# Kernel optimization log

Measured on AMD Instinct MI355X. Metric: run time of the kernel, lower is better.

Reference implementation:

```python
import jax, jax.numpy as jnp
import numpy as np

N_POINTS = 8192
N_TOPICS = 64
B = 524288


def setup_inputs() -> dict:
    key = jax.random.key(0)
    k1, k2, k3, k4 = jax.random.split(key, 4)
    pij = jax.random.uniform(k1, (B,), dtype=jnp.float32, minval=1e-6, maxval=1.0)
    i = jax.random.randint(k2, (B,), 0, N_POINTS, dtype=jnp.int64)
    j = jax.random.randint(k3, (B,), 0, N_POINTS, dtype=jnp.int64)
    W = jax.random.normal(k4, (N_POINTS, N_TOPICS), dtype=jnp.float32)  # nn.Embedding weight
    return {"pij": pij, "i": i, "j": j, "W": W}


def reference(pij, i, j, W):
    # pairwise squared distances over ALL points, via the gram trick
    # (avoids materializing the [n, n, d] broadcasted tensor of the torch code)
    sq = jnp.sum(W * W, axis=1)                       # [n]
    d2 = sq[:, None] + sq[None, :] - 2.0 * (W @ W.T)  # [n, n]
    d2 = jnp.maximum(d2, 0.0)                         # numerical floor (exact math is >= 0)
    n = W.shape[0]
    # Cauchy kernel partition: sum_{k,l} 1/(1+d2) minus the n diagonal ones
    part = jnp.sum(1.0 / (1.0 + d2)) - jnp.asarray(n, d2.dtype)
    xi = W[i]                                         # [B, d]
    xj = W[j]                                         # [B, d]
    # FAITHFUL to source: (1 + diff^2).sum(1) adds 1 per dim => n_topics + ||xi-xj||^2
    num = 1.0 / jnp.sum(1.0 + (xi - xj) ** 2, axis=1)  # [B]
    qij = num / part
    loss_kld = pij * (jnp.log(pij) - jnp.log(qij))
    return jnp.sum(loss_kld)
```

## Files before the change

kernel.cpp:

```cpp
#include <hip/hip_runtime.h>
#include <math.h>

#define NPOINTS   8192
#define NDIM      64
#define TILE      128
#define NT2       64
#define NBLK      2080
#define NPAIRB    1040
#define NPW       (NPAIRB * 4)
#define GRID      3120

#define WS_W16   0
#define WS_SQ    262144
#define WS_PARTA 270336
#define WS_A1P   272416
#define WS_A3P   273456

typedef __attribute__((ext_vector_type(8))) short bf16x8;
typedef __attribute__((ext_vector_type(4))) float f32x4;

__device__ inline unsigned short f2bf(float f) {
    unsigned u = __float_as_uint(f);
    u += 0x7FFFu + ((u >> 16) & 1u);
    return (unsigned short)(u >> 16);
}
__device__ inline float bflo(unsigned u) { return __uint_as_float(u << 16); }
__device__ inline float bfhi(unsigned u) { return __uint_as_float(u & 0xFFFF0000u); }

__global__ __launch_bounds__(256) void prep_kernel(const float* __restrict__ W,
                                                   float* __restrict__ sq,
                                                   unsigned* __restrict__ W16) {
    int wid  = (blockIdx.x * 256 + threadIdx.x) >> 6;
    int lane = threadIdx.x & 63;
    float v = W[wid * NDIM + lane];
    float s = v * v;
    #pragma unroll
    for (int m = 32; m >= 1; m >>= 1) s += __shfl_xor(s, m, 64);
    if (lane == 0) sq[wid] = s;
    unsigned bf   = f2bf(v);
    unsigned peer = (unsigned)__shfl_xor((int)bf, 1, 64);
    if ((lane & 1) == 0)
        W16[wid * 32 + (lane >> 1)] = (bf & 0xFFFFu) | (peer << 16);
}

__global__ __launch_bounds__(256) void fused_kernel(const unsigned* __restrict__ W16,
                                                    const float* __restrict__ sq,
                                                    const float* __restrict__ pij,
                                                    const int* __restrict__ ii,
                                                    const int* __restrict__ jj,
                                                    int nb,
                                                    float* __restrict__ partA,
                                                    float* __restrict__ a1p,
                                                    float* __restrict__ a3p) {
    __shared__ float red[8];
    int zb = blockIdx.x;
    int t = threadIdx.x, w = t >> 6, lane = t & 63;

    if ((zb % 3) < 2) {
        int z = (zb / 3) * 2 + (zb % 3);
        int by = (int)((129.0 - sqrt(16641.0 - 8.0 * (double)z)) * 0.5);
        while (by * NT2 - by * (by - 1) / 2 > z) --by;
        while ((by + 1) * NT2 - (by + 1) * by / 2 <= z) ++by;
        int bx = by + (z - (by * NT2 - by * (by - 1) / 2));

        int wm = w >> 1, wn = w & 1, quad = lane >> 4, l15 = lane & 15;
        int a0 = by * TILE, b0 = bx * TILE;

        float4 base1[4];
        float  sqb[4];
        {
            int arow = a0 + wm * 64 + quad * 4;
            #pragma unroll
            for (int tm = 0; tm < 4; ++tm) {
                float4 v = *(const float4*)(sq + arow + tm * 16);
                base1[tm] = (float4){1.0f + v.x, 1.0f + v.y, 1.0f + v.z, 1.0f + v.w};
            }
            int bcol = b0 + wn * 64 + l15;
            #pragma unroll
            for (int tn = 0; tn < 4; ++tn) sqb[tn] = sq[bcol + tn * 16];
        }

        f32x4 acc[4][4];
        #pragma unroll
        for (int i = 0; i < 4; ++i)
            #pragma unroll
            for (int j = 0; j < 4; ++j) acc[i][j] = (f32x4){0.f, 0.f, 0.f, 0.f};

        const unsigned* Arow = W16 + (a0 + wm * 64 + l15) * 32;
        const unsigned* Brow = W16 + (b0 + wn * 64 + l15) * 32;
        #pragma unroll
        for (int h = 0; h < 2; ++h) {
            bf16x8 af[4], bfr[4];
            #pragma unroll
            for (int tm = 0; tm < 4; ++tm)
                af[tm] = *(const bf16x8*)(Arow + tm * 16 * 32 + h * 16 + quad * 4);
            #pragma unroll
            for (int tn = 0; tn < 4; ++tn)
                bfr[tn] = *(const bf16x8*)(Brow + tn * 16 * 32 + h * 16 + quad * 4);
            #pragma unroll
            for (int tm = 0; tm < 4; ++tm)
                #pragma unroll
                for (int tn = 0; tn < 4; ++tn)
                    acc[tm][tn] = __builtin_amdgcn_mfma_f32_16x16x32_bf16(af[tm], bfr[tn],
                                                                          acc[tm][tn], 0, 0, 0);
        }

        float ssum = 0.f;
        if (bx > by) {
            #pragma unroll
            for (int tn = 0; tn < 4; ++tn) {
                float c0 = sqb[tn];
                #pragma unroll
                for (int tm = 0; tm < 4; ++tm) {
                    ssum += __builtin_amdgcn_rcpf(fmaf(acc[tm][tn][0], -2.0f, base1[tm].x + c0));
                    ssum += __builtin_amdgcn_rcpf(fmaf(acc[tm][tn][1], -2.0f, base1[tm].y + c0));
                    ssum += __builtin_amdgcn_rcpf(fmaf(acc[tm][tn][2], -2.0f, base1[tm].z + c0));
                    ssum += __builtin_amdgcn_rcpf(fmaf(acc[tm][tn][3], -2.0f, base1[tm].w + c0));
                }
            }
        } else {
            int quad4 = quad * 4;
            #pragma unroll
            for (int tn = 0; tn < 4; ++tn) {
                int cl = wn * 64 + tn * 16 + l15;
                float c0 = sqb[tn];
                float b4[4];
                #pragma unroll
                for (int tm = 0; tm < 4; ++tm) {
                    b4[0] = base1[tm].x; b4[1] = base1[tm].y;
                    b4[2] = base1[tm].z; b4[3] = base1[tm].w;
                    #pragma unroll
                    for (int r = 0; r < 4; ++r) {
                        int rl = wm * 64 + tm * 16 + quad4 + r;
                        float inv = __builtin_amdgcn_rcpf(fmaf(acc[tm][tn][r], -2.0f, b4[r] + c0));
                        ssum += (cl > rl) ? inv : 0.f;
                    }
                }
            }
        }
        #pragma unroll
        for (int m = 32; m >= 1; m >>= 1) ssum += __shfl_xor(ssum, m, 64);
        if (lane == 0) red[w] = ssum;
        __syncthreads();
        if (t == 0) partA[z] = red[0] + red[1] + red[2] + red[3];
    } else {
        int pb = zb / 3;
        int pw = pb * 4 + w;
        int g = lane >> 3;
        int s = lane & 7;
        float a1 = 0.f, a3 = 0.f;

        #pragma unroll 2
        for (int p0 = pw * 16; p0 < nb; p0 += NPW * 16) {
            int  pA = p0 + g,        pB = p0 + 8 + g;
            bool okA = pA < nb,      okB = pB < nb;
            int  cA = okA ? pA : 0,  cB = okB ? pB : 0;
            int   iA = ii[cA], jA = jj[cA];
            int   iB = ii[cB], jB = jj[cB];
            float pvA = pij[cA], pvB = pij[cB];
            uint4 xiA = *(const uint4*)(W16 + iA * 32 + s * 4);
            uint4 xjA = *(const uint4*)(W16 + jA * 32 + s * 4);
            uint4 xiB = *(const uint4*)(W16 + iB * 32 + s * 4);
            uint4 xjB = *(const uint4*)(W16 + jB * 32 + s * 4);
            float sA = sq[iA] + sq[jA];
            float sB = sq[iB] + sq[jB];

            float dA, dB;
            {
                dA = bflo(xiA.x) * bflo(xjA.x);
                dA = fmaf(bfhi(xiA.x), bfhi(xjA.x), dA);
                dA = fmaf(bflo(xiA.y), bflo(xjA.y), dA);
                dA = fmaf(bfhi(xiA.y), bfhi(xjA.y), dA);
                dA = fmaf(bflo(xiA.z), bflo(xjA.z), dA);
                dA = fmaf(bfhi(xiA.z), bfhi(xjA.z), dA);
                dA = fmaf(bflo(xiA.w), bflo(xjA.w), dA);
                dA = fmaf(bfhi(xiA.w), bfhi(xjA.w), dA);
            }
            {
                dB = bflo(xiB.x) * bflo(xjB.x);
                dB = fmaf(bfhi(xiB.x), bfhi(xjB.x), dB);
                dB = fmaf(bflo(xiB.y), bflo(xjB.y), dB);
                dB = fmaf(bfhi(xiB.y), bfhi(xjB.y), dB);
                dB = fmaf(bflo(xiB.z), bflo(xjB.z), dB);
                dB = fmaf(bfhi(xiB.z), bfhi(xjB.z), dB);
                dB = fmaf(bflo(xiB.w), bflo(xjB.w), dB);
                dB = fmaf(bfhi(xiB.w), bfhi(xjB.w), dB);
            }
            #pragma unroll
            for (int m = 1; m <= 4; m <<= 1) {
                dA += __shfl_xor(dA, m, 64);
                dB += __shfl_xor(dB, m, 64);
            }
            float vA = fmaf(dA, -2.0f, sA);
            float vB = fmaf(dB, -2.0f, sB);
            float tA = pvA * __logf(pvA * ((float)NDIM + vA));
            float tB = pvB * __logf(pvB * ((float)NDIM + vB));
            a1 += okA ? tA : 0.f;  a3 += okA ? pvA : 0.f;
            a1 += okB ? tB : 0.f;  a3 += okB ? pvB : 0.f;
        }
        #pragma unroll
        for (int m = 32; m >= 1; m >>= 1) {
            a1 += __shfl_xor(a1, m, 64);
            a3 += __shfl_xor(a3, m, 64);
        }
        if (lane == 0) { red[w] = a1 * 0.125f; red[4 + w] = a3 * 0.125f; }
        __syncthreads();
        if (t == 0) {
            a1p[pb] = red[0] + red[1] + red[2] + red[3];
            a3p[pb] = red[4] + red[5] + red[6] + red[7];
        }
    }
}

__global__ __launch_bounds__(256) void final_kernel(const float* __restrict__ partA,
                                                    const float* __restrict__ a1p,
                                                    const float* __restrict__ a3p,
                                                    float* __restrict__ out) {
    __shared__ double r1[256], r2[256], r3[256];
    int t = threadIdx.x;
    double dpart = 0.0, d1 = 0.0, d3 = 0.0;
    for (int k = t; k < NBLK; k += 256) dpart += (double)partA[k];
    for (int k = t; k < NPAIRB; k += 256) { d1 += (double)a1p[k]; d3 += (double)a3p[k]; }
    r1[t] = dpart; r2[t] = d1; r3[t] = d3;
    __syncthreads();
    for (int s = 128; s >= 1; s >>= 1) {
        if (t < s) { r1[t] += r1[t + s]; r2[t] += r2[t + s]; r3[t] += r3[t + s]; }
        __syncthreads();
    }
    if (t == 0) {
        double part = 2.0 * r1[0];
        out[0] = (float)(r2[0] + r3[0] * log(part));
    }
}

extern "C" void kernel_launch(void* const* d_in, const int* in_sizes, int n_in,
                              void* d_out, int out_size, void* d_ws, size_t ws_size,
                              hipStream_t stream) {
    const float* pij = (const float*)d_in[0];
    const int*   ii  = (const int*)d_in[1];
    const int*   jj  = (const int*)d_in[2];
    const float* W   = (const float*)d_in[3];
    float* out = (float*)d_out;
    float* ws  = (float*)d_ws;

    unsigned* W16   = (unsigned*)ws + WS_W16;
    float*    sqv   = ws + WS_SQ;
    float*    partA = ws + WS_PARTA;
    float*    a1p   = ws + WS_A1P;
    float*    a3p   = ws + WS_A3P;

    int nb = in_sizes[0];

    prep_kernel<<<NPOINTS / 4, 256, 0, stream>>>(W, sqv, W16);
    fused_kernel<<<GRID, 256, 0, stream>>>(W16, sqv, pij, ii, jj, nb, partA, a1p, a3p);
    final_kernel<<<1, 256, 0, stream>>>(partA, a1p, a3p, out);
}
```

Measured before the change: 110.9 us.

## Gather embeddings as fp8 and compute direct squared differences for pair loss

The prep kernel now also packs W into fp8 (e4m3) rows. The pair branch gathers 8-byte fp8 chunks instead of 16-byte bf16 ones and computes the sum of squared differences directly, which drops the sq lookups and the gram-trick subtraction. The block interleave changes from 2:1 to 1:1, doubling the number of pair blocks to spread the gather work. This halves the gather bytes per pair, but fp8 precision is coarse and may push the loss sum outside tolerance.

```diff
diff --git a/kernel.cpp b/kernel.cpp
--- a/kernel.cpp
+++ b/kernel.cpp
@@ -6,32 +6,38 @@
 #define TILE      128
 #define NT2       64
 #define NBLK      2080
-#define NPAIRB    1040
+#define NPAIRB    2080
 #define NPW       (NPAIRB * 4)
-#define GRID      3120
+#define GRID      (NBLK + NPAIRB)
 
 #define WS_W16   0
-#define WS_SQ    262144
-#define WS_PARTA 270336
-#define WS_A1P   272416
-#define WS_A3P   273456
+#define WS_W8    262144
+#define WS_SQ    393216
+#define WS_PARTA 401408
+#define WS_A1P   403488
+#define WS_A3P   405568
 
 typedef __attribute__((ext_vector_type(8))) short bf16x8;
 typedef __attribute__((ext_vector_type(4))) float f32x4;
+typedef __attribute__((ext_vector_type(2))) float f32x2;
 
 __device__ inline unsigned short f2bf(float f) {
     unsigned u = __float_as_uint(f);
     u += 0x7FFFu + ((u >> 16) & 1u);
     return (unsigned short)(u >> 16);
 }
-__device__ inline float bflo(unsigned u) { return __uint_as_float(u << 16); }
-__device__ inline float bfhi(unsigned u) { return __uint_as_float(u & 0xFFFF0000u); }
+template <bool HI>
+__device__ inline f32x2 cvt2(unsigned dw) {
+    return __builtin_amdgcn_cvt_pk_f32_fp8((int)dw, HI);
+}
 
 __global__ __launch_bounds__(256) void prep_kernel(const float* __restrict__ W,
                                                    float* __restrict__ sq,
-                                                   unsigned* __restrict__ W16) {
-    int wid  = (blockIdx.x * 256 + threadIdx.x) >> 6;
-    int lane = threadIdx.x & 63;
+                                                   unsigned* __restrict__ W16,
+                                                   unsigned* __restrict__ W8) {
+    int t    = threadIdx.x;
+    int wid  = (blockIdx.x * 256 + t) >> 6;
+    int lane = t & 63;
     float v = W[wid * NDIM + lane];
     float s = v * v;
     #pragma unroll
@@ -41,9 +47,16 @@
     unsigned peer = (unsigned)__shfl_xor((int)bf, 1, 64);
     if ((lane & 1) == 0)
         W16[wid * 32 + (lane >> 1)] = (bf & 0xFFFFu) | (peer << 16);
+    if (t < 64) {
+        float4 x = *(const float4*)(W + blockIdx.x * 256 + t * 4);
+        int lo = __builtin_amdgcn_cvt_pk_fp8_f32(x.x, x.y, 0, false);
+        int dw = __builtin_amdgcn_cvt_pk_fp8_f32(x.z, x.w, lo, true);
+        W8[blockIdx.x * 64 + t] = (unsigned)dw;
+    }
 }
 
 __global__ __launch_bounds__(256) void fused_kernel(const unsigned* __restrict__ W16,
+                                                    const unsigned* __restrict__ W8,
                                                     const float* __restrict__ sq,
                                                     const float* __restrict__ pij,
                                                     const int* __restrict__ ii,
@@ -56,8 +69,8 @@
     int zb = blockIdx.x;
     int t = threadIdx.x, w = t >> 6, lane = t & 63;
 
-    if ((zb % 3) < 2) {
-        int z = (zb / 3) * 2 + (zb % 3);
+    if ((zb & 1) == 0) {
+        int z = zb >> 1;
         int by = (int)((129.0 - sqrt(16641.0 - 8.0 * (double)z)) * 0.5);
         while (by * NT2 - by * (by - 1) / 2 > z) --by;
         while ((by + 1) * NT2 - (by + 1) * by / 2 <= z) ++by;
@@ -144,10 +157,11 @@
         __syncthreads();
         if (t == 0) partA[z] = red[0] + red[1] + red[2] + red[3];
     } else {
-        int pb = zb / 3;
+        int pb = zb >> 1;
         int pw = pb * 4 + w;
         int g = lane >> 3;
         int s = lane & 7;
+        const uint2* W8v = (const uint2*)W8;
         float a1 = 0.f, a3 = 0.f;
 
         #pragma unroll 2
@@ -158,41 +172,33 @@
             int   iA = ii[cA], jA = jj[cA];
             int   iB = ii[cB], jB = jj[cB];
             float pvA = pij[cA], pvB = pij[cB];
-            uint4 xiA = *(const uint4*)(W16 + iA * 32 + s * 4);
-            uint4 xjA = *(const uint4*)(W16 + jA * 32 + s * 4);
-            uint4 xiB = *(const uint4*)(W16 + iB * 32 + s * 4);
-            uint4 xjB = *(const uint4*)(W16 + jB * 32 + s * 4);
-            float sA = sq[iA] + sq[jA];
-            float sB = sq[iB] + sq[jB];
-
-            float dA, dB;
+            uint2 xa = W8v[iA * 8 + s], ya = W8v[jA * 8 + s];
+            uint2 xb = W8v[iB * 8 + s], yb = W8v[jB * 8 + s];
+
+            float vA, vB;
             {
-                dA = bflo(xiA.x) * bflo(xjA.x);
-                dA = fmaf(bfhi(xiA.x), bfhi(xjA.x), dA);
-                dA = fmaf(bflo(xiA.y), bflo(xjA.y), dA);
-                dA = fmaf(bfhi(xiA.y), bfhi(xjA.y), dA);
-                dA = fmaf(bflo(xiA.z), bflo(xjA.z), dA);
-                dA = fmaf(bfhi(xiA.z), bfhi(xjA.z), dA);
-                dA = fmaf(bflo(xiA.w), bflo(xjA.w), dA);
-                dA = fmaf(bfhi(xiA.w), bfhi(xjA.w), dA);
+                f32x2 d0 = cvt2<false>(xa.x) - cvt2<false>(ya.x);
+                f32x2 d1 = cvt2<true >(xa.x) - cvt2<true >(ya.x);
+                f32x2 d2 = cvt2<false>(xa.y) - cvt2<false>(ya.y);
+                f32x2 d3 = cvt2<true >(xa.y) - cvt2<true >(ya.y);
+                f32x2 acc2 = d0 * d0;
+                acc2 += d1 * d1; acc2 += d2 * d2; acc2 += d3 * d3;
+                vA = acc2.x + acc2.y;
             }
             {
-                dB = bflo(xiB.x) * bflo(xjB.x);
-                dB = fmaf(bfhi(xiB.x), bfhi(xjB.x), dB);
-                dB = fmaf(bflo(xiB.y), bflo(xjB.y), dB);
-                dB = fmaf(bfhi(xiB.y), bfhi(xjB.y), dB);
-                dB = fmaf(bflo(xiB.z), bflo(xjB.z), dB);
-                dB = fmaf(bfhi(xiB.z), bfhi(xjB.z), dB);
-                dB = fmaf(bflo(xiB.w), bflo(xjB.w), dB);
-                dB = fmaf(bfhi(xiB.w), bfhi(xjB.w), dB);
+                f32x2 d0 = cvt2<false>(xb.x) - cvt2<false>(yb.x);
+                f32x2 d1 = cvt2<true >(xb.x) - cvt2<true >(yb.x);
+                f32x2 d2 = cvt2<false>(xb.y) - cvt2<false>(yb.y);
+                f32x2 d3 = cvt2<true >(xb.y) - cvt2<true >(yb.y);
+                f32x2 acc2 = d0 * d0;
+                acc2 += d1 * d1; acc2 += d2 * d2; acc2 += d3 * d3;
+                vB = acc2.x + acc2.y;
             }
             #pragma unroll
             for (int m = 1; m <= 4; m <<= 1) {
-                dA += __shfl_xor(dA, m, 64);
-                dB += __shfl_xor(dB, m, 64);
-            }
-            float vA = fmaf(dA, -2.0f, sA);
-            float vB = fmaf(dB, -2.0f, sB);
+                vA += __shfl_xor(vA, m, 64);
+                vB += __shfl_xor(vB, m, 64);
+            }
             float tA = pvA * __logf(pvA * ((float)NDIM + vA));
             float tB = pvB * __logf(pvB * ((float)NDIM + vB));
             a1 += okA ? tA : 0.f;  a3 += okA ? pvA : 0.f;
@@ -244,6 +250,7 @@
     float* ws  = (float*)d_ws;
 
     unsigned* W16   = (unsigned*)ws + WS_W16;
+    unsigned* W8    = (unsigned*)ws + WS_W8;
     float*    sqv   = ws + WS_SQ;
     float*    partA = ws + WS_PARTA;
     float*    a1p   = ws + WS_A1P;
@@ -251,7 +258,7 @@
 
     int nb = in_sizes[0];
 
-    prep_kernel<<<NPOINTS / 4, 256, 0, stream>>>(W, sqv, W16);
-    fused_kernel<<<GRID, 256, 0, stream>>>(W16, sqv, pij, ii, jj, nb, partA, a1p, a3p);
+    prep_kernel<<<NPOINTS / 4, 256, 0, stream>>>(W, sqv, W16, W8);
+    fused_kernel<<<GRID, 256, 0, stream>>>(W16, W8, sqv, pij, ii, jj, nb, partA, a1p, a3p);
     final_kernel<<<1, 256, 0, stream>>>(partA, a1p, a3p, out);
 }
```

Result: slower. 118.0 us (+6.5%).
